# Performance work log

Hardware: AMD Instinct MI355X
Metric: run time of the kernel (lower is better)

The kernel has to match this reference:

```python
import jax, jax.numpy as jnp
import numpy as np

B, T, C, H = 4, 2048, 1024, 16
D = C // H  # head dim = 64


def setup_inputs() -> dict:
    key = jax.random.key(0)
    ks = jax.random.split(key, 5)
    s = 1.0 / np.sqrt(C)
    return {
        "x": jax.random.normal(ks[0], (B, T, C), dtype=jnp.float32),
        "Wq": jax.random.normal(ks[1], (C, C), dtype=jnp.float32) * s,
        "bq": jnp.zeros((C,), dtype=jnp.float32),
        "Wk": jax.random.normal(ks[2], (C, C), dtype=jnp.float32) * s,
        "bk": jnp.zeros((C,), dtype=jnp.float32),
        "Wv": jax.random.normal(ks[3], (C, C), dtype=jnp.float32) * s,
        "bv": jnp.zeros((C,), dtype=jnp.float32),
        "Wp": jax.random.normal(ks[4], (C, C), dtype=jnp.float32) * s,
        "bp": jnp.zeros((C,), dtype=jnp.float32),
    }


def reference(x, Wq, bq, Wk, bk, Wv, bv, Wp, bp):
    Bb, Tt, Cc = x.shape
    # QKV projections (torch Linear: y = x @ W.T + b)
    q = (x @ Wq.T + bq).reshape(Bb, Tt, H, D).transpose(0, 2, 1, 3)  # [B,H,T,D]
    k = (x @ Wk.T + bk).reshape(Bb, Tt, H, D).transpose(0, 2, 1, 3)
    v = (x @ Wv.T + bv).reshape(Bb, Tt, H, D).transpose(0, 2, 1, 3)
    att = jnp.einsum("bhqd,bhkd->bhqk", q, k) / jnp.sqrt(jnp.float32(D))
    causal = jnp.tril(jnp.ones((Tt, Tt), dtype=bool))
    att = jnp.where(causal[None, None], att, -jnp.inf)
    att = jax.nn.softmax(att, axis=-1)
    y = jnp.einsum("bhqk,bhkd->bhqd", att, v)  # [B,H,T,D]
    y = y.transpose(0, 2, 1, 3).reshape(Bb, Tt, Cc)
    return y @ Wp.T + bp
```

## Files before the change

kernel.cpp:

```cpp
#include <hip/hip_runtime.h>

typedef unsigned short u16;
typedef unsigned int u32;

typedef __attribute__((ext_vector_type(4))) float f32x4;
typedef __attribute__((ext_vector_type(8))) short bf16x8;


__device__ inline u16 f2b(float f) {
  union { float f; u32 u; } x; x.f = f;
  u32 u = x.u;
  u32 r = (u + 0x7fffu + ((u >> 16) & 1u)) >> 16;
  return (u16)r;
}

__device__ inline u32 cvtpk(float lo, float hi) {
  u32 r;
  asm("v_cvt_pk_bf16_f32 %0, %1, %2" : "=v"(r) : "v"(lo), "v"(hi));
  return r;
}

__device__ inline void gload_lds16(const void* g, void* l) {
  __builtin_amdgcn_global_load_lds(
      (const __attribute__((address_space(1))) u32*)g,
      (__attribute__((address_space(3))) u32*)l, 16, 0, 0);
}


__global__ __launch_bounds__(256) void cvt_bf16(const float* __restrict__ src,
                                                u16* __restrict__ dst, int n4) {
  int i = blockIdx.x * blockDim.x + threadIdx.x;
  if (i >= n4) return;
  float4 v = ((const float4*)src)[i];
  ushort4 o;
  o.x = f2b(v.x); o.y = f2b(v.y); o.z = f2b(v.z); o.w = f2b(v.w);
  ((ushort4*)dst)[i] = o;
}

__global__ __launch_bounds__(256) void cvt_w4(const float* __restrict__ w0,
                                              const float* __restrict__ w1,
                                              const float* __restrict__ w2,
                                              const float* __restrict__ w3,
                                              u16* o0, u16* o1, u16* o2, u16* o3) {
  int m = blockIdx.x >> 10;
  const float* s = (m == 0) ? w0 : (m == 1) ? w1 : (m == 2) ? w2 : w3;
  u16* d = (m == 0) ? o0 : (m == 1) ? o1 : (m == 2) ? o2 : o3;
  int i = (blockIdx.x & 1023) * 256 + threadIdx.x;
  float4 v = ((const float4*)s)[i];
  ushort4 o;
  o.x = f2b(v.x); o.y = f2b(v.y); o.z = f2b(v.z); o.w = f2b(v.w);
  ((ushort4*)d)[i] = o;
}


template <int MODE>
__global__ __launch_bounds__(256) void gemm_bt(const u16* __restrict__ A,
                                               const u16* __restrict__ W,
                                               const float* __restrict__ bias,
                                               float* __restrict__ outF,
                                               u16* __restrict__ outB,
                                               int M, int N, int K,
                                               float oscale) {
  __shared__ u16 sA[128 * 32];
  __shared__ u16 sB[128 * 32];

  const int t = threadIdx.x;
  const int lane = t & 63;
  const int w = t >> 6;
  const int wr = w >> 1, wc = w & 1;
  const int lr = lane & 15, lg = lane >> 4;

  int bid = blockIdx.y * 8 + blockIdx.x;
  int swz = (bid & 7) * 64 + (bid >> 3);
  const int mBase = (swz >> 3) * 128;
  const int nBase = (swz & 7) * 128;

  f32x4 zero = {0.f, 0.f, 0.f, 0.f};
  f32x4 acc[4][4];
#pragma unroll
  for (int i = 0; i < 4; ++i)
#pragma unroll
    for (int j = 0; j < 4; ++j) acc[i][j] = zero;

  const int rA = t >> 2;
  const int cA = (t & 3) * 8;

  for (int k0 = 0; k0 < K; k0 += 32) {
#pragma unroll
    for (int i = 0; i < 2; ++i) {
      gload_lds16(A + (size_t)(mBase + i * 64 + rA) * K + k0 + cA,
                  &sA[i * 2048 + t * 8]);
      gload_lds16(W + (size_t)(nBase + i * 64 + rA) * K + k0 + cA,
                  &sB[i * 2048 + t * 8]);
    }
    __syncthreads();

    bf16x8 af[4], bf[4];
#pragma unroll
    for (int i = 0; i < 4; ++i)
      af[i] = *(const bf16x8*)&sA[(wr * 64 + i * 16 + lr) * 32 + lg * 8];
#pragma unroll
    for (int j = 0; j < 4; ++j)
      bf[j] = *(const bf16x8*)&sB[(wc * 64 + j * 16 + lr) * 32 + lg * 8];

#pragma unroll
    for (int i = 0; i < 4; ++i)
#pragma unroll
      for (int j = 0; j < 4; ++j)
        acc[i][j] = __builtin_amdgcn_mfma_f32_16x16x32_bf16(af[i], bf[j],
                                                            acc[i][j], 0, 0, 0);
    __syncthreads();
  }

#pragma unroll
  for (int i = 0; i < 4; ++i) {
    int row = mBase + wr * 64 + i * 16 + lg * 4;
#pragma unroll
    for (int j = 0; j < 4; ++j) {
      int col = nBase + wc * 64 + j * 16 + lr;
      float bv = bias[col];
      if (MODE == 2) {
        int b = row >> 11, tp = row & 2047;
        int h = col >> 6, d = col & 63;
        ushort4 o;
        o.x = f2b((acc[i][j][0] + bv) * oscale);
        o.y = f2b((acc[i][j][1] + bv) * oscale);
        o.z = f2b((acc[i][j][2] + bv) * oscale);
        o.w = f2b((acc[i][j][3] + bv) * oscale);
        *(ushort4*)(outB + ((size_t)((b * 16 + h) * 64 + d)) * 2048 + tp) = o;
      } else {
#pragma unroll
        for (int r = 0; r < 4; ++r) {
          float v = (acc[i][j][r] + bv) * oscale;
          if (MODE == 0) {
            outF[(size_t)(row + r) * N + col] = v;
          } else {
            int m = row + r;
            int b = m >> 11, tp = m & 2047;
            int h = col >> 6, d = col & 63;
            outB[(((size_t)(b * 16 + h) * 2048) + tp) * 64 + d] = f2b(v);
          }
        }
      }
    }
  }
}


__global__ __launch_bounds__(512) void attn_fwd(const u16* __restrict__ qg,
                                                const u16* __restrict__ kg,
                                                const u16* __restrict__ vtg,
                                                u16* __restrict__ yg) {
  __shared__ u16 sK[2][64 * 64];
  __shared__ u16 sVt[2][64 * 64];

  const int t = threadIdx.x;
  const int lane = t & 63;
  const int w = t >> 6;
  const int lr = lane & 15, lg = lane >> 4;

  int bid0 = blockIdx.y * 8 + blockIdx.x;
  int swzb = (bid0 & 7) * 64 + (bid0 >> 3);
  const int bh = swzb >> 3;
  const int pair = swzb & 7;
  const size_t base = (size_t)bh * 2048 * 64;

  const u32* ks = (const u32*)(kg + base);
  const u32* vs = (const u32*)(vtg + base);

  u32 kreg[4], vreg[4];
#pragma unroll
  for (int e = 0; e < 4; ++e) {
    int p = t + e * 512;
    int row = p >> 5, dp = p & 31;
    kreg[e] = ks[p];
    vreg[e] = vs[row * 1024 + dp];
  }

  f32x4 zero = {0.f, 0.f, 0.f, 0.f};
  const int b = bh >> 4, h = bh & 15;

  for (int half = 0; half < 2; ++half) {
    const int qt = half ? pair : 15 - pair;
    const int nkt = 2 * qt + 2;
    const int wq0 = qt * 128 + w * 16;
    const int qrow = wq0 + lr;

    bf16x8 qf[2];
#pragma unroll
    for (int kk = 0; kk < 2; ++kk)
      qf[kk] = *(const bf16x8*)(qg + base + (size_t)qrow * 64 + kk * 32 + lg * 8);

    f32x4 accO[4];
#pragma unroll
    for (int n = 0; n < 4; ++n) accO[n] = zero;
    float mrun = -1e30f, lrun = 0.f;

    for (int kt = 0; kt < nkt; ++kt) {
      char* kb_ = (char*)&sK[kt & 1][0];
      char* vb_ = (char*)&sVt[kt & 1][0];

#pragma unroll
      for (int e = 0; e < 4; ++e) {
        int p = t + e * 512;
        int row = p >> 5, dp = p & 31;
        int off = row * 128 + ((dp * 4) ^ ((row & 7) << 4));
        *(u32*)(kb_ + off) = kreg[e];
        *(u32*)(vb_ + off) = vreg[e];
      }

      int nextT = (kt + 1 < nkt) ? kt + 1 : (half == 0 ? 0 : -1);
      if (nextT >= 0) {
        const u32* kn = ks + (size_t)nextT * 2048;
        const u32* vn = vs + nextT * 32;
#pragma unroll
        for (int e = 0; e < 4; ++e) {
          int p = t + e * 512;
          int row = p >> 5, dp = p & 31;
          kreg[e] = kn[p];
          vreg[e] = vn[row * 1024 + dp];
        }
      }

      __syncthreads();

      f32x4 s[4];
      __builtin_amdgcn_s_setprio(1);
#pragma unroll
      for (int n = 0; n < 4; ++n) {
        f32x4 a = zero;
#pragma unroll
        for (int kk = 0; kk < 2; ++kk) {
          bf16x8 kf = *(const bf16x8*)(kb_ + (n * 16 + lr) * 128 +
                                       ((kk * 64 + lg * 16) ^ ((lr & 7) << 4)));
          a = __builtin_amdgcn_mfma_f32_16x16x32_bf16(kf, qf[kk], a, 0, 0, 0);
        }
        s[n] = a;
      }
      __builtin_amdgcn_s_setprio(0);

      if (kt * 64 + 63 > wq0) {
#pragma unroll
        for (int n = 0; n < 4; ++n) {
          int key0 = kt * 64 + n * 16 + lg * 4;
#pragma unroll
          for (int r = 0; r < 4; ++r)
            s[n][r] = (key0 + r <= qrow) ? s[n][r] : -1e30f;
        }
      }

      float pmax = -1e30f;
#pragma unroll
      for (int n = 0; n < 4; ++n)
        pmax = fmaxf(pmax, fmaxf(fmaxf(s[n][0], s[n][1]), fmaxf(s[n][2], s[n][3])));
      pmax = fmaxf(pmax, __shfl_xor(pmax, 16));
      pmax = fmaxf(pmax, __shfl_xor(pmax, 32));

      const bool full = __any(pmax > mrun + 8.f);
      float mnew = full ? fmaxf(mrun, pmax) : mrun;
      float corr = full ? exp2f(mrun - mnew) : 1.f;
      mrun = mnew;

      float psum = 0.f;
      u32 pk[4][2];
#pragma unroll
      for (int n = 0; n < 4; ++n) {
        float p0 = exp2f(s[n][0] - mnew);
        float p1 = exp2f(s[n][1] - mnew);
        float p2 = exp2f(s[n][2] - mnew);
        float p3 = exp2f(s[n][3] - mnew);
        psum += (p0 + p1) + (p2 + p3);
        pk[n][0] = cvtpk(p0, p1);
        pk[n][1] = cvtpk(p2, p3);
      }
      psum += __shfl_xor(psum, 16);
      psum += __shfl_xor(psum, 32);

      if (full) {
        lrun = lrun * corr + psum;
        float c4[4];
#pragma unroll
        for (int r = 0; r < 4; ++r) c4[r] = __shfl(corr, lg * 4 + r);
#pragma unroll
        for (int n = 0; n < 4; ++n)
#pragma unroll
          for (int r = 0; r < 4; ++r) accO[n][r] *= c4[r];
      } else {
        lrun += psum;
      }

      const bool hi = (lg >> 1) & 1;
#pragma unroll
      for (int kk = 0; kk < 2; ++kk) {
        u32 g[4];
#pragma unroll
        for (int r = 0; r < 4; ++r) {
          const int rh = r >> 1, rl = r & 1;
          u32 give = ((lg & 1) ^ rh) ? pk[2 * kk + 1][rl] : pk[2 * kk][rl];
          int srcLane = ((lg & 1) * 2 + ((lg >> 1) ^ rh)) * 16 + lr;
          g[r] = (u32)__shfl((int)give, srcLane);
        }
        union { u32 u[4]; bf16x8 v; } pu;
        pu.u[0] = hi ? g[2] : g[0];
        pu.u[1] = hi ? g[3] : g[1];
        pu.u[2] = hi ? g[0] : g[2];
        pu.u[3] = hi ? g[1] : g[3];
        bf16x8 pf = pu.v;
        __builtin_amdgcn_s_setprio(1);
#pragma unroll
        for (int n = 0; n < 4; ++n) {
          bf16x8 vf = *(const bf16x8*)(vb_ + (n * 16 + lr) * 128 +
                                       ((kk * 64 + lg * 16) ^ ((lr & 7) << 4)));
          accO[n] = __builtin_amdgcn_mfma_f32_16x16x32_bf16(pf, vf, accO[n], 0, 0, 0);
        }
        __builtin_amdgcn_s_setprio(0);
      }
    }

#pragma unroll
    for (int r = 0; r < 4; ++r) {
      float linv = 1.f / __shfl(lrun, lg * 4 + r);
      int trow = qt * 128 + w * 16 + lg * 4 + r;
      size_t rowOff = ((size_t)b * 2048 + trow) * 1024 + h * 64;
#pragma unroll
      for (int n = 0; n < 4; ++n)
        yg[rowOff + n * 16 + lr] = f2b(accO[n][r] * linv);
    }
  }
}


extern "C" void kernel_launch(void* const* d_in, const int* in_sizes, int n_in,
                              void* d_out, int out_size, void* d_ws, size_t ws_size,
                              hipStream_t stream) {
  const float* x  = (const float*)d_in[0];
  const float* Wq = (const float*)d_in[1];
  const float* bq = (const float*)d_in[2];
  const float* Wk = (const float*)d_in[3];
  const float* bk = (const float*)d_in[4];
  const float* Wv = (const float*)d_in[5];
  const float* bv = (const float*)d_in[6];
  const float* Wp = (const float*)d_in[7];
  const float* bp = (const float*)d_in[8];
  float* out = (float*)d_out;

  char* ws = (char*)d_ws;
  u16* xb  = (u16*)(ws);
  u16* wqb = (u16*)(ws + (16u << 20));
  u16* wkb = (u16*)(ws + (18u << 20));
  u16* wvb = (u16*)(ws + (20u << 20));
  u16* wpb = (u16*)(ws + (22u << 20));
  u16* qb  = (u16*)(ws + (24u << 20));
  u16* kb  = (u16*)(ws + (40u << 20));
  u16* vtb = (u16*)(ws + (56u << 20));
  u16* yb  = (u16*)(ws + (72u << 20));

  const float SCL = 0.18033688011112042f;

  cvt_bf16<<<8192, 256, 0, stream>>>(x, xb, 2097152);
  cvt_w4<<<4096, 256, 0, stream>>>(Wq, Wk, Wv, Wp, wqb, wkb, wvb, wpb);

  gemm_bt<1><<<dim3(8, 64), 256, 0, stream>>>(xb, wqb, bq, nullptr, qb, 8192, 1024, 1024, SCL);
  gemm_bt<1><<<dim3(8, 64), 256, 0, stream>>>(xb, wkb, bk, nullptr, kb, 8192, 1024, 1024, 1.f);
  gemm_bt<2><<<dim3(8, 64), 256, 0, stream>>>(xb, wvb, bv, nullptr, vtb, 8192, 1024, 1024, 1.f);

  attn_fwd<<<dim3(8, 64), 512, 0, stream>>>(qb, kb, vtb, yb);

  gemm_bt<0><<<dim3(8, 64), 256, 0, stream>>>(yb, wpb, bp, out, nullptr, 8192, 1024, 1024, 1.f);
}
```

Measured before the change: 210.7 us.

## Fuse conversion and QKV GEMM launches, enlarge attention key tile to 128

The two bf16 conversion kernels are merged into one launch. The three separate Q/K/V projection GEMMs become a single 24x64-grid GEMM that treats the concatenated weights as one N=3072 matrix and picks bias, scale and output layout per column block. The attention kernel now processes 128-key tiles instead of 64, which halves the loop iterations and barriers per query tile, at the cost of more registers (launch bounds set to 4 waves per SIMD), double the LDS footprint and a wider V-transpose swizzle. The combined GEMM also gives the GPU more blocks per launch and removes launch gaps.

Result: slower. 222.9 us (+5.8%).

```diff
diff --git a/kernel.cpp b/kernel.cpp
--- a/kernel.cpp
+++ b/kernel.cpp
@@ -27,25 +27,25 @@
 }
 
 
-__global__ __launch_bounds__(256) void cvt_bf16(const float* __restrict__ src,
-                                                u16* __restrict__ dst, int n4) {
-  int i = blockIdx.x * blockDim.x + threadIdx.x;
-  if (i >= n4) return;
-  float4 v = ((const float4*)src)[i];
-  ushort4 o;
-  o.x = f2b(v.x); o.y = f2b(v.y); o.z = f2b(v.z); o.w = f2b(v.w);
-  ((ushort4*)dst)[i] = o;
-}
-
-__global__ __launch_bounds__(256) void cvt_w4(const float* __restrict__ w0,
-                                              const float* __restrict__ w1,
-                                              const float* __restrict__ w2,
-                                              const float* __restrict__ w3,
-                                              u16* o0, u16* o1, u16* o2, u16* o3) {
-  int m = blockIdx.x >> 10;
-  const float* s = (m == 0) ? w0 : (m == 1) ? w1 : (m == 2) ? w2 : w3;
-  u16* d = (m == 0) ? o0 : (m == 1) ? o1 : (m == 2) ? o2 : o3;
-  int i = (blockIdx.x & 1023) * 256 + threadIdx.x;
+__global__ __launch_bounds__(256) void cvt_all(const float* __restrict__ x,
+                                               const float* __restrict__ w0,
+                                               const float* __restrict__ w1,
+                                               const float* __restrict__ w2,
+                                               const float* __restrict__ w3,
+                                               u16* __restrict__ xo,
+                                               u16* __restrict__ wo) {
+  int b = blockIdx.x;
+  const float* s;
+  u16* d;
+  int i;
+  if (b < 8192) {
+    s = x; d = xo; i = b * 256 + threadIdx.x;
+  } else {
+    int m = (b - 8192) >> 10;
+    s = (m == 0) ? w0 : (m == 1) ? w1 : (m == 2) ? w2 : w3;
+    d = wo + (size_t)m * 1048576;
+    i = ((b - 8192) & 1023) * 256 + threadIdx.x;
+  }
   float4 v = ((const float4*)s)[i];
   ushort4 o;
   o.x = f2b(v.x); o.y = f2b(v.y); o.z = f2b(v.z); o.w = f2b(v.w);
@@ -53,27 +53,29 @@
 }
 
 
-template <int MODE>
-__global__ __launch_bounds__(256) void gemm_bt(const u16* __restrict__ A,
-                                               const u16* __restrict__ W,
-                                               const float* __restrict__ bias,
-                                               float* __restrict__ outF,
-                                               u16* __restrict__ outB,
-                                               int M, int N, int K,
-                                               float oscale) {
+__global__ __launch_bounds__(256) void gemm_qkv(const u16* __restrict__ A,
+                                                const u16* __restrict__ W,
+                                                const float* __restrict__ bq,
+                                                const float* __restrict__ bk,
+                                                const float* __restrict__ bv,
+                                                u16* __restrict__ outQ,
+                                                u16* __restrict__ outK,
+                                                u16* __restrict__ outVt,
+                                                float qscale) {
   __shared__ u16 sA[128 * 32];
   __shared__ u16 sB[128 * 32];
 
+  const int K = 1024;
   const int t = threadIdx.x;
   const int lane = t & 63;
   const int w = t >> 6;
   const int wr = w >> 1, wc = w & 1;
   const int lr = lane & 15, lg = lane >> 4;
 
-  int bid = blockIdx.y * 8 + blockIdx.x;
-  int swz = (bid & 7) * 64 + (bid >> 3);
-  const int mBase = (swz >> 3) * 128;
-  const int nBase = (swz & 7) * 128;
+  int bid = blockIdx.y * 24 + blockIdx.x;
+  int swz = (bid & 7) * 192 + (bid >> 3);
+  const int mBase = (swz / 24) * 128;
+  const int nBase = (swz % 24) * 128;
 
   f32x4 zero = {0.f, 0.f, 0.f, 0.f};
   f32x4 acc[4][4];
@@ -112,6 +114,95 @@
     __syncthreads();
   }
 
+  const int mode = nBase >> 10;
+  const float* bias = (mode == 0) ? bq : (mode == 1) ? bk : bv;
+  const float scl = (mode == 0) ? qscale : 1.f;
+
+#pragma unroll
+  for (int i = 0; i < 4; ++i) {
+    int row = mBase + wr * 64 + i * 16 + lg * 4;
+    int b = row >> 11, tp = row & 2047;
+#pragma unroll
+    for (int j = 0; j < 4; ++j) {
+      int col = nBase + wc * 64 + j * 16 + lr;
+      int ncol = col & 1023;
+      int h = ncol >> 6, dd = ncol & 63;
+      float bv_ = bias[ncol];
+      if (mode == 2) {
+        ushort4 o;
+        o.x = f2b(acc[i][j][0] + bv_);
+        o.y = f2b(acc[i][j][1] + bv_);
+        o.z = f2b(acc[i][j][2] + bv_);
+        o.w = f2b(acc[i][j][3] + bv_);
+        *(ushort4*)(outVt + ((size_t)((b * 16 + h) * 64 + dd)) * 2048 + tp) = o;
+      } else {
+        u16* ob = (mode == 0) ? outQ : outK;
+#pragma unroll
+        for (int r = 0; r < 4; ++r)
+          ob[(((size_t)(b * 16 + h) * 2048) + tp + r) * 64 + dd] =
+              f2b((acc[i][j][r] + bv_) * scl);
+      }
+    }
+  }
+}
+
+
+__global__ __launch_bounds__(256) void gemm_proj(const u16* __restrict__ A,
+                                                 const u16* __restrict__ W,
+                                                 const float* __restrict__ bias,
+                                                 float* __restrict__ outF) {
+  __shared__ u16 sA[128 * 32];
+  __shared__ u16 sB[128 * 32];
+
+  const int K = 1024, N = 1024;
+  const int t = threadIdx.x;
+  const int lane = t & 63;
+  const int w = t >> 6;
+  const int wr = w >> 1, wc = w & 1;
+  const int lr = lane & 15, lg = lane >> 4;
+
+  int bid = blockIdx.y * 8 + blockIdx.x;
+  int swz = (bid & 7) * 64 + (bid >> 3);
+  const int mBase = (swz >> 3) * 128;
+  const int nBase = (swz & 7) * 128;
+
+  f32x4 zero = {0.f, 0.f, 0.f, 0.f};
+  f32x4 acc[4][4];
+#pragma unroll
+  for (int i = 0; i < 4; ++i)
+#pragma unroll
+    for (int j = 0; j < 4; ++j) acc[i][j] = zero;
+
+  const int rA = t >> 2;
+  const int cA = (t & 3) * 8;
+
+  for (int k0 = 0; k0 < K; k0 += 32) {
+#pragma unroll
+    for (int i = 0; i < 2; ++i) {
+      gload_lds16(A + (size_t)(mBase + i * 64 + rA) * K + k0 + cA,
+                  &sA[i * 2048 + t * 8]);
+      gload_lds16(W + (size_t)(nBase + i * 64 + rA) * K + k0 + cA,
+                  &sB[i * 2048 + t * 8]);
+    }
+    __syncthreads();
+
+    bf16x8 af[4], bf[4];
+#pragma unroll
+    for (int i = 0; i < 4; ++i)
+      af[i] = *(const bf16x8*)&sA[(wr * 64 + i * 16 + lr) * 32 + lg * 8];
+#pragma unroll
+    for (int j = 0; j < 4; ++j)
+      bf[j] = *(const bf16x8*)&sB[(wc * 64 + j * 16 + lr) * 32 + lg * 8];
+
+#pragma unroll
+    for (int i = 0; i < 4; ++i)
+#pragma unroll
+      for (int j = 0; j < 4; ++j)
+        acc[i][j] = __builtin_amdgcn_mfma_f32_16x16x32_bf16(af[i], bf[j],
+                                                            acc[i][j], 0, 0, 0);
+    __syncthreads();
+  }
+
 #pragma unroll
   for (int i = 0; i < 4; ++i) {
     int row = mBase + wr * 64 + i * 16 + lg * 4;
@@ -119,40 +210,20 @@
     for (int j = 0; j < 4; ++j) {
       int col = nBase + wc * 64 + j * 16 + lr;
       float bv = bias[col];
-      if (MODE == 2) {
-        int b = row >> 11, tp = row & 2047;
-        int h = col >> 6, d = col & 63;
-        ushort4 o;
-        o.x = f2b((acc[i][j][0] + bv) * oscale);
-        o.y = f2b((acc[i][j][1] + bv) * oscale);
-        o.z = f2b((acc[i][j][2] + bv) * oscale);
-        o.w = f2b((acc[i][j][3] + bv) * oscale);
-        *(ushort4*)(outB + ((size_t)((b * 16 + h) * 64 + d)) * 2048 + tp) = o;
-      } else {
-#pragma unroll
-        for (int r = 0; r < 4; ++r) {
-          float v = (acc[i][j][r] + bv) * oscale;
-          if (MODE == 0) {
-            outF[(size_t)(row + r) * N + col] = v;
-          } else {
-            int m = row + r;
-            int b = m >> 11, tp = m & 2047;
-            int h = col >> 6, d = col & 63;
-            outB[(((size_t)(b * 16 + h) * 2048) + tp) * 64 + d] = f2b(v);
-          }
-        }
-      }
-    }
-  }
-}
-
-
-__global__ __launch_bounds__(512) void attn_fwd(const u16* __restrict__ qg,
-                                                const u16* __restrict__ kg,
-                                                const u16* __restrict__ vtg,
-                                                u16* __restrict__ yg) {
-  __shared__ u16 sK[2][64 * 64];
-  __shared__ u16 sVt[2][64 * 64];
+#pragma unroll
+      for (int r = 0; r < 4; ++r)
+        outF[(size_t)(row + r) * N + col] = acc[i][j][r] + bv;
+    }
+  }
+}
+
+
+__global__ __launch_bounds__(512, 4) void attn_fwd(const u16* __restrict__ qg,
+                                                   const u16* __restrict__ kg,
+                                                   const u16* __restrict__ vtg,
+                                                   u16* __restrict__ yg) {
+  __shared__ u16 sK[2][128 * 64];
+  __shared__ u16 sVt[2][64 * 128];
 
   const int t = threadIdx.x;
   const int lane = t & 63;
@@ -168,21 +239,21 @@
   const u32* ks = (const u32*)(kg + base);
   const u32* vs = (const u32*)(vtg + base);
 
-  u32 kreg[4], vreg[4];
-#pragma unroll
-  for (int e = 0; e < 4; ++e) {
+  u32 kreg[8], vreg[8];
+#pragma unroll
+  for (int e = 0; e < 8; ++e) {
     int p = t + e * 512;
-    int row = p >> 5, dp = p & 31;
     kreg[e] = ks[p];
-    vreg[e] = vs[row * 1024 + dp];
+    vreg[e] = vs[(p >> 6) * 1024 + (p & 63)];
   }
 
   f32x4 zero = {0.f, 0.f, 0.f, 0.f};
   const int b = bh >> 4, h = bh & 15;
+  int tc = 0;
 
   for (int half = 0; half < 2; ++half) {
     const int qt = half ? pair : 15 - pair;
-    const int nkt = 2 * qt + 2;
+    const int nkt = qt + 1;
     const int wq0 = qt * 128 + w * 16;
     const int qrow = wq0 + lr;
 
@@ -196,38 +267,37 @@
     for (int n = 0; n < 4; ++n) accO[n] = zero;
     float mrun = -1e30f, lrun = 0.f;
 
-    for (int kt = 0; kt < nkt; ++kt) {
-      char* kb_ = (char*)&sK[kt & 1][0];
-      char* vb_ = (char*)&sVt[kt & 1][0];
-
-#pragma unroll
-      for (int e = 0; e < 4; ++e) {
+    for (int kt = 0; kt < nkt; ++kt, ++tc) {
+      char* kb_ = (char*)&sK[tc & 1][0];
+      char* vb_ = (char*)&sVt[tc & 1][0];
+
+#pragma unroll
+      for (int e = 0; e < 8; ++e) {
         int p = t + e * 512;
-        int row = p >> 5, dp = p & 31;
-        int off = row * 128 + ((dp * 4) ^ ((row & 7) << 4));
-        *(u32*)(kb_ + off) = kreg[e];
-        *(u32*)(vb_ + off) = vreg[e];
+        int kr = p >> 5, kd = p & 31;
+        *(u32*)(kb_ + kr * 128 + ((kd * 4) ^ ((kr & 7) << 4))) = kreg[e];
+        int vr = p >> 6, vd = p & 63;
+        *(u32*)(vb_ + vr * 256 + ((vd * 4) ^ ((vr & 15) << 4))) = vreg[e];
       }
 
       int nextT = (kt + 1 < nkt) ? kt + 1 : (half == 0 ? 0 : -1);
       if (nextT >= 0) {
-        const u32* kn = ks + (size_t)nextT * 2048;
-        const u32* vn = vs + nextT * 32;
-#pragma unroll
-        for (int e = 0; e < 4; ++e) {
+        const u32* kn = ks + (size_t)nextT * 4096;
+        const u32* vn = vs + nextT * 64;
+#pragma unroll
+        for (int e = 0; e < 8; ++e) {
           int p = t + e * 512;
-          int row = p >> 5, dp = p & 31;
           kreg[e] = kn[p];
-          vreg[e] = vn[row * 1024 + dp];
+          vreg[e] = vn[(p >> 6) * 1024 + (p & 63)];
         }
       }
 
       __syncthreads();
 
-      f32x4 s[4];
+      f32x4 s[8];
       __builtin_amdgcn_s_setprio(1);
 #pragma unroll
-      for (int n = 0; n < 4; ++n) {
+      for (int n = 0; n < 8; ++n) {
         f32x4 a = zero;
 #pragma unroll
         for (int kk = 0; kk < 2; ++kk) {
@@ -239,10 +309,10 @@
       }
       __builtin_amdgcn_s_setprio(0);
 
-      if (kt * 64 + 63 > wq0) {
-#pragma unroll
-        for (int n = 0; n < 4; ++n) {
-          int key0 = kt * 64 + n * 16 + lg * 4;
+      if (kt == qt) {
+#pragma unroll
+        for (int n = 0; n < 8; ++n) {
+          int key0 = kt * 128 + n * 16 + lg * 4;
 #pragma unroll
           for (int r = 0; r < 4; ++r)
             s[n][r] = (key0 + r <= qrow) ? s[n][r] : -1e30f;
@@ -251,7 +321,7 @@
 
       float pmax = -1e30f;
 #pragma unroll
-      for (int n = 0; n < 4; ++n)
+      for (int n = 0; n < 8; ++n)
         pmax = fmaxf(pmax, fmaxf(fmaxf(s[n][0], s[n][1]), fmaxf(s[n][2], s[n][3])));
       pmax = fmaxf(pmax, __shfl_xor(pmax, 16));
       pmax = fmaxf(pmax, __shfl_xor(pmax, 32));
@@ -262,9 +332,9 @@
       mrun = mnew;
 
       float psum = 0.f;
-      u32 pk[4][2];
-#pragma unroll
-      for (int n = 0; n < 4; ++n) {
+      u32 pk[8][2];
+#pragma unroll
+      for (int n = 0; n < 8; ++n) {
         float p0 = exp2f(s[n][0] - mnew);
         float p1 = exp2f(s[n][1] - mnew);
         float p2 = exp2f(s[n][2] - mnew);
@@ -291,7 +361,7 @@
 
       const bool hi = (lg >> 1) & 1;
 #pragma unroll
-      for (int kk = 0; kk < 2; ++kk) {
+      for (int kk = 0; kk < 4; ++kk) {
         u32 g[4];
 #pragma unroll
         for (int r = 0; r < 4; ++r) {
@@ -309,8 +379,8 @@
         __builtin_amdgcn_s_setprio(1);
 #pragma unroll
         for (int n = 0; n < 4; ++n) {
-          bf16x8 vf = *(const bf16x8*)(vb_ + (n * 16 + lr) * 128 +
-                                       ((kk * 64 + lg * 16) ^ ((lr & 7) << 4)));
+          bf16x8 vf = *(const bf16x8*)(vb_ + (n * 16 + lr) * 256 +
+                                       ((kk * 64 + lg * 16) ^ ((lr & 15) << 4)));
           accO[n] = __builtin_amdgcn_mfma_f32_16x16x32_bf16(pf, vf, accO[n], 0, 0, 0);
         }
         __builtin_amdgcn_s_setprio(0);
@@ -347,8 +417,6 @@
   char* ws = (char*)d_ws;
   u16* xb  = (u16*)(ws);
   u16* wqb = (u16*)(ws + (16u << 20));
-  u16* wkb = (u16*)(ws + (18u << 20));
-  u16* wvb = (u16*)(ws + (20u << 20));
   u16* wpb = (u16*)(ws + (22u << 20));
   u16* qb  = (u16*)(ws + (24u << 20));
   u16* kb  = (u16*)(ws + (40u << 20));
@@ -357,14 +425,12 @@
 
   const float SCL = 0.18033688011112042f;
 
-  cvt_bf16<<<8192, 256, 0, stream>>>(x, xb, 2097152);
-  cvt_w4<<<4096, 256, 0, stream>>>(Wq, Wk, Wv, Wp, wqb, wkb, wvb, wpb);
-
-  gemm_bt<1><<<dim3(8, 64), 256, 0, stream>>>(xb, wqb, bq, nullptr, qb, 8192, 1024, 1024, SCL);
-  gemm_bt<1><<<dim3(8, 64), 256, 0, stream>>>(xb, wkb, bk, nullptr, kb, 8192, 1024, 1024, 1.f);
-  gemm_bt<2><<<dim3(8, 64), 256, 0, stream>>>(xb, wvb, bv, nullptr, vtb, 8192, 1024, 1024, 1.f);
+  cvt_all<<<12288, 256, 0, stream>>>(x, Wq, Wk, Wv, Wp, xb, wqb);
+
+  gemm_qkv<<<dim3(24, 64), 256, 0, stream>>>(xb, wqb, bq, bk, bv,
+                                             qb, kb, vtb, SCL);
 
   attn_fwd<<<dim3(8, 64), 512, 0, stream>>>(qb, kb, vtb, yb);
 
-  gemm_bt<0><<<dim3(8, 64), 256, 0, stream>>>(yb, wpb, bp, out, nullptr, 8192, 1024, 1024, 1.f);
-}
+  gemm_proj<<<dim3(8, 64), 256, 0, stream>>>(yb, wpb, bp, out);
+}
```
